# Kernel optimization log

Measured on AMD Instinct MI355X. Metric: run time of the kernel, lower is better.

## Reference

```python
import jax, jax.numpy as jnp
import numpy as np

B, L, IN, DM, DS, DC, EXP = 4, 1024, 256, 1024, 16, 4, 2
DI = EXP * DM            # d_inner = 2048
DTR = (DM + 15) // 16    # dt_rank = 64


def setup_inputs() -> dict:
    key = jax.random.key(0)
    ks = jax.random.split(key, 10)
    s = lambda k, sh, sc: jax.random.normal(k, sh, jnp.float32) * sc
    return {
        "x": s(ks[0], (B, L, IN), 1.0),
        "W_emb": s(ks[1], (DM, IN), IN ** -0.5),
        "b_emb": jnp.zeros((DM,), jnp.float32),
        "in_proj_w": s(ks[2], (2 * DI, DM), DM ** -0.5),
        "conv_w": s(ks[3], (DI, 1, DC), DC ** -0.5),
        "conv_b": jnp.zeros((DI,), jnp.float32),
        "x_proj_w": s(ks[4], (DTR + 2 * DS, DI), DI ** -0.5),
        "dt_proj_w": s(ks[5], (DI, DTR), DTR ** -0.5),
        "dt_proj_b": s(ks[6], (DI,), 0.1),
        "A_log": jnp.tile(jnp.log(jnp.arange(1, DS + 1, dtype=jnp.float32)), (DI, 1)),
        "D": jnp.ones((DI,), jnp.float32),
        "out_proj_w": s(ks[7], (DM, DI), DI ** -0.5),
        "fc_w": s(ks[8], (1, DM), DM ** -0.5),
        "fc_b": jnp.zeros((1,), jnp.float32),
    }


def _forward(x, W_emb, b_emb, in_proj_w, conv_w, conv_b, x_proj_w,
             dt_proj_w, dt_proj_b, A_log, D, out_proj_w, fc_w, fc_b):
    h = x @ W_emb.T + b_emb                      # [B,L,DM] input embedding
    xz = h @ in_proj_w.T                         # [B,L,2*DI]
    u, z = jnp.split(xz, 2, axis=-1)             # each [B,L,DI]
    # causal depthwise conv over time (pad left d_conv-1)
    uc = jax.lax.conv_general_dilated(
        u.transpose(0, 2, 1), conv_w, (1,), [(DC - 1, 0)],
        dimension_numbers=('NCH', 'OIH', 'NCH'), feature_group_count=DI)
    u = jax.nn.silu(uc.transpose(0, 2, 1) + conv_b)   # [B,L,DI]
    xdbl = u @ x_proj_w.T                        # [B,L,DTR+2*DS]
    dt, Bm, Cm = jnp.split(xdbl, [DTR, DTR + DS], axis=-1)
    delta = jax.nn.softplus(dt @ dt_proj_w.T + dt_proj_b)  # [B,L,DI]
    A = -jnp.exp(A_log)                          # [DI,DS]

    def step(hst, ins):
        d_t, B_t, C_t, u_t = ins                 # [B,DI],[B,DS],[B,DS],[B,DI]
        dA = jnp.exp(d_t[..., None] * A)         # [B,DI,DS]
        hst = dA * hst + (d_t * u_t)[..., None] * B_t[:, None, :]
        y = jnp.einsum('bds,bs->bd', hst, C_t)
        return hst, y

    h0 = jnp.zeros((B, DI, DS), u.dtype)
    _, ys = jax.lax.scan(step, h0, (delta.transpose(1, 0, 2),
                                    Bm.transpose(1, 0, 2),
                                    Cm.transpose(1, 0, 2),
                                    u.transpose(1, 0, 2)))
    y = ys.transpose(1, 0, 2) + D * u            # [B,L,DI] with D skip
    y = y * jax.nn.silu(z)                       # gate
    out = y @ out_proj_w.T                       # [B,L,DM]
    return out[:, -1, :] @ fc_w.T + fc_b         # [B,1]


def reference(x, W_emb, b_emb, in_proj_w, conv_w, conv_b, x_proj_w,
              dt_proj_w, dt_proj_b, A_log, D, out_proj_w, fc_w, fc_b):
    return _forward(x, W_emb, b_emb, in_proj_w, conv_w, conv_b, x_proj_w,
                    dt_proj_w, dt_proj_b, A_log, D, out_proj_w, fc_w, fc_b)
```

## Files before the change

### kernel.cpp

```cpp
#include <hip/hip_runtime.h>
#include <cstddef>
#include <cstdint>

namespace {

typedef _Float16 half8 __attribute__((ext_vector_type(8)));
typedef _Float16 half4 __attribute__((ext_vector_type(4)));
typedef float f32x4 __attribute__((ext_vector_type(4)));

constexpr int Bn   = 4;
constexpr int Ln   = 1024;
constexpr int INn  = 256;
constexpr int DMn  = 1024;
constexpr int DSn  = 16;
constexpr int DCn  = 4;
constexpr int DIn  = 2048;
constexpr int DTRn = 64;
constexpr int XPW  = DTRn + DSn;
constexpr int NCHUNK = 64;
constexpr int CHUNK  = Ln / NCHUNK;
constexpr int WCH  = 32;
constexpr int ML   = Bn * Ln;

__device__ __forceinline__ float silu_(float x) { return x / (1.f + __expf(-x)); }
__device__ __forceinline__ float softplus_(float x) {
    return fmaxf(x, 0.f) + __logf(1.f + __expf(-fabsf(x)));
}

__global__ __launch_bounds__(256)
void prep_mega(const float* __restrict__ x, _Float16* __restrict__ xh,
               const float* __restrict__ ip, _Float16* __restrict__ iph,
               const float* __restrict__ dtw, _Float16* __restrict__ dtwh,
               const float* __restrict__ W_emb, _Float16* __restrict__ W_embT,
               const float* __restrict__ x_proj, _Float16* __restrict__ xp_h,
               const float* __restrict__ fc_w, const float* __restrict__ out_w,
               float* __restrict__ wp,
               const float* __restrict__ b_emb, float* __restrict__ badd,
               const float* __restrict__ fc_b, float* __restrict__ out) {
    __shared__ float tile[32][33];
    const int bid = blockIdx.x, tid = threadIdx.x;
    if (bid < 4096) {
        const int n = bid;
        const float4 v = ((const float4*)ip)[n * 256 + tid];
        ((half4*)iph)[n * 256 + tid] =
            half4{(_Float16)v.x, (_Float16)v.y, (_Float16)v.z, (_Float16)v.w};
        const float4 bv = ((const float4*)b_emb)[tid];
        float s = v.x * bv.x + v.y * bv.y + v.z * bv.z + v.w * bv.w;
        for (int off = 32; off > 0; off >>= 1) s += __shfl_down(s, off);
        if ((tid & 63) == 0) tile[0][tid >> 6] = s;
        __syncthreads();
        if (tid == 0) badd[n] = tile[0][0] + tile[0][1] + tile[0][2] + tile[0][3];
    } else if (bid < 5248) {
        const float* in; _Float16* outp; int i;
        if (bid < 5120) { in = x;   outp = xh;   i = (bid - 4096) * 256 + tid; }
        else            { in = dtw; outp = dtwh; i = (bid - 5120) * 256 + tid; }
        const float4 v = ((const float4*)in)[i];
        ((half4*)outp)[i] = half4{(_Float16)v.x, (_Float16)v.y, (_Float16)v.z, (_Float16)v.w};
    } else if (bid < 5504) {
        const int bx = bid - 5248;
        const int m0 = (bx & 31) * 32, c0 = (bx >> 5) * 32;
        const int lc = tid & 31, lr = tid >> 5;
        #pragma unroll
        for (int ph = 0; ph < 4; ++ph)
            tile[lr + ph * 8][lc] = W_emb[(size_t)(m0 + lr + ph * 8) * INn + c0 + lc];
        __syncthreads();
        #pragma unroll
        for (int ph = 0; ph < 4; ++ph)
            W_embT[(size_t)(c0 + lr + ph * 8) * DMn + m0 + lc] = (_Float16)tile[lc][lr + ph * 8];
    } else if (bid < 5760) {
        const int i = (bid - 5504) * 256 + tid;
        const int r = i >> 9;
        const int c4 = i & 511;
        half4 h;
        if (r < XPW) {
            const float4 v = ((const float4*)(x_proj + (size_t)r * DIn))[c4];
            h = half4{(_Float16)v.x, (_Float16)v.y, (_Float16)v.z, (_Float16)v.w};
        } else {
            h = half4{(_Float16)0.f, (_Float16)0.f, (_Float16)0.f, (_Float16)0.f};
        }
        ((half4*)(xp_h + (size_t)r * DIn))[c4] = h;
    } else if (bid < 6016) {
        const int bx = bid - 5760;
        const int d = (bx & 7) * 256 + tid;
        const int c = bx >> 3;
        const int mstep = DMn / WCH;
        float s = 0.f;
        for (int m = c * mstep; m < (c + 1) * mstep; ++m)
            s += fc_w[m] * out_w[(size_t)m * DIn + d];
        wp[(size_t)c * DIn + d] = s;
    } else {
        if (tid < Bn) out[tid] = fc_b[0];
    }
}

__global__ __launch_bounds__(256)
void skgemm2(const _Float16* __restrict__ A, int lda,
             const _Float16* __restrict__ Bw, int ldb,
             float* __restrict__ P, int N, int Kc) {
    __shared__ _Float16 As[128 * 32];
    __shared__ _Float16 Bs[128 * 32];
    const int tid  = threadIdx.x;
    const int lane = tid & 63, wid = tid >> 6;
    const int wm = wid >> 1, wn = wid & 1;
    const int sk = blockIdx.x;
    const int m0 = blockIdx.y * 128;
    const int n0 = blockIdx.z * 128;
    const int M  = gridDim.y * 128;

    f32x4 acc[4][4] = {};
    const int kbeg = sk * Kc;
    for (int k0 = kbeg; k0 < kbeg + Kc; k0 += 32) {
        #pragma unroll
        for (int i = 0; i < 2; ++i) {
            const int off = tid * 16 + i * 4096;
            const int row = off >> 6;
            const int ch  = (off & 63) >> 1;
            __builtin_amdgcn_global_load_lds(
                (const __attribute__((address_space(1))) void*)(A + (size_t)(m0 + row) * lda + k0 + ch),
                (__attribute__((address_space(3))) void*)(&As[off >> 1]), 16, 0, 0);
            __builtin_amdgcn_global_load_lds(
                (const __attribute__((address_space(1))) void*)(Bw + (size_t)(n0 + row) * ldb + k0 + ch),
                (__attribute__((address_space(3))) void*)(&Bs[off >> 1]), 16, 0, 0);
        }
        __syncthreads();
        const int ar = lane & 15;
        const int kq = (lane >> 4) * 8;
        half8 af[4], bf[4];
        #pragma unroll
        for (int i = 0; i < 4; ++i)
            af[i] = *(const half8*)&As[(wm * 64 + i * 16 + ar) * 32 + kq];
        #pragma unroll
        for (int j = 0; j < 4; ++j)
            bf[j] = *(const half8*)&Bs[(wn * 64 + j * 16 + ar) * 32 + kq];
        #pragma unroll
        for (int i = 0; i < 4; ++i)
            #pragma unroll
            for (int j = 0; j < 4; ++j)
                acc[i][j] = __builtin_amdgcn_mfma_f32_16x16x32_f16(af[i], bf[j], acc[i][j], 0, 0, 0);
        __syncthreads();
    }
    const int cr = (lane >> 4) * 4;
    const int cn = lane & 15;
    #pragma unroll
    for (int i = 0; i < 4; ++i)
        #pragma unroll
        for (int j = 0; j < 4; ++j) {
            const int n = n0 + wn * 64 + j * 16 + cn;
            if (n < N) {
                #pragma unroll
                for (int r = 0; r < 4; ++r) {
                    const int m = m0 + wm * 64 + i * 16 + cr + r;
                    P[((size_t)sk * M + m) * N + n] = acc[i][j][r];
                }
            }
        }
}

__global__ __launch_bounds__(256)
void skcomb(const float* __restrict__ P, _Float16* __restrict__ out, int total, int nsk) {
    const int i = blockIdx.x * 256 + threadIdx.x;
    if (i >= total) return;
    float s = 0.f;
    for (int k = 0; k < nsk; ++k) s += P[(size_t)k * total + i];
    out[i] = (_Float16)s;
}

__global__ __launch_bounds__(256)
void skcombB_clast(const float* __restrict__ P, _Float16* __restrict__ dtBh,
                   const _Float16* __restrict__ u, const float* __restrict__ x_proj,
                   float* __restrict__ Clast) {
    const int bid = blockIdx.x, tid = threadIdx.x;
    if (bid < 1280) {
        const int i = bid * 256 + tid;
        float s = 0.f;
        #pragma unroll
        for (int k = 0; k < 8; ++k) s += P[(size_t)k * (ML * XPW) + i];
        dtBh[i] = (_Float16)s;
    } else {
        const int wave = tid >> 6, lane = tid & 63;
        const int task = (bid - 1280) * 4 + wave;
        const int s_idx = task & 15, b = task >> 4;
        const _Float16* ur = u + ((size_t)b * Ln + (Ln - 1)) * DIn;
        const float* w = x_proj + (size_t)(XPW + s_idx) * DIn;
        float s = 0.f;
        for (int k = lane; k < DIn; k += 64) s += (float)ur[k] * w[k];
        for (int off = 32; off > 0; off >>= 1) s += __shfl_down(s, off);
        if (lane == 0) Clast[b * DSn + s_idx] = s;
    }
}

__global__ __launch_bounds__(256)
void hgemm_upre(const _Float16* __restrict__ A, const _Float16* __restrict__ Bw,
                const float* __restrict__ bias, _Float16* __restrict__ Ch) {
    __shared__ _Float16 As[128 * 32];
    __shared__ _Float16 Bs[128 * 32];
    const int tid  = threadIdx.x;
    const int lane = tid & 63, wid = tid >> 6;
    const int wm = wid >> 1, wn = wid & 1;
    const int m0 = blockIdx.y * 128, n0 = blockIdx.x * 128;

    f32x4 acc[4][4] = {};
    for (int k0 = 0; k0 < INn; k0 += 32) {
        #pragma unroll
        for (int i = 0; i < 2; ++i) {
            const int off = tid * 16 + i * 4096;
            const int row = off >> 6;
            const int ch  = (off & 63) >> 1;
            __builtin_amdgcn_global_load_lds(
                (const __attribute__((address_space(1))) void*)(A + (size_t)(m0 + row) * INn + k0 + ch),
                (__attribute__((address_space(3))) void*)(&As[off >> 1]), 16, 0, 0);
            __builtin_amdgcn_global_load_lds(
                (const __attribute__((address_space(1))) void*)(Bw + (size_t)(n0 + row) * INn + k0 + ch),
                (__attribute__((address_space(3))) void*)(&Bs[off >> 1]), 16, 0, 0);
        }
        __syncthreads();
        const int ar = lane & 15;
        const int kq = (lane >> 4) * 8;
        half8 af[4], bf[4];
        #pragma unroll
        for (int i = 0; i < 4; ++i)
            af[i] = *(const half8*)&As[(wm * 64 + i * 16 + ar) * 32 + kq];
        #pragma unroll
        for (int j = 0; j < 4; ++j)
            bf[j] = *(const half8*)&Bs[(wn * 64 + j * 16 + ar) * 32 + kq];
        #pragma unroll
        for (int i = 0; i < 4; ++i)
            #pragma unroll
            for (int j = 0; j < 4; ++j)
                acc[i][j] = __builtin_amdgcn_mfma_f32_16x16x32_f16(af[i], bf[j], acc[i][j], 0, 0, 0);
        __syncthreads();
    }
    const int cr = (lane >> 4) * 4;
    const int cn = lane & 15;
    #pragma unroll
    for (int i = 0; i < 4; ++i)
        #pragma unroll
        for (int j = 0; j < 4; ++j) {
            const int n = n0 + wn * 64 + j * 16 + cn;
            #pragma unroll
            for (int r = 0; r < 4; ++r) {
                const int m = m0 + wm * 64 + i * 16 + cr + r;
                Ch[(size_t)m * DIn + n] = (_Float16)(acc[i][j][r] + bias[n]);
            }
        }
}

__global__ __launch_bounds__(256)
void conv_zlast(const _Float16* __restrict__ upre, const float* __restrict__ cw,
                const float* __restrict__ cb, _Float16* __restrict__ uh,
                const float* __restrict__ x, const _Float16* __restrict__ Wfh,
                const float* __restrict__ badd, float* __restrict__ zlast) {
    const int tid = threadIdx.x;
    const int bid = blockIdx.x;
    if (bid < 1024) {
        const int b  = bid >> 8;
        const int t0 = (bid & 255) * 4;
        const int d0 = tid * 8;
        const size_t rowbase = ((size_t)b * Ln + t0) * DIn + d0;
        half8 hzero;
        #pragma unroll
        for (int q = 0; q < 8; ++q) hzero[q] = (_Float16)0.f;
        half8 rows[7];
        if (t0 >= 3) {
            #pragma unroll
            for (int r = 0; r < 7; ++r)
                rows[r] = *(const half8*)(upre + rowbase + (ptrdiff_t)(r - 3) * DIn);
        } else {
            #pragma unroll
            for (int r = 0; r < 7; ++r) {
                const int t = t0 - 3 + r;
                rows[r] = (t >= 0) ? *(const half8*)(upre + rowbase + (ptrdiff_t)(r - 3) * DIn) : hzero;
            }
        }
        f32x4 cwq[8];
        float cbv[8];
        #pragma unroll
        for (int q = 0; q < 8; ++q) {
            cwq[q] = *(const f32x4*)(cw + (size_t)(d0 + q) * DCn);
            cbv[q] = cb[d0 + q];
        }
        #pragma unroll
        for (int s = 0; s < 4; ++s) {
            half8 o;
            #pragma unroll
            for (int q = 0; q < 8; ++q) {
                float acc = cbv[q];
                #pragma unroll
                for (int j = 0; j < DCn; ++j) acc += (float)rows[s + j][q] * cwq[q][j];
                o[q] = (_Float16)silu_(acc);
            }
            *(half8*)(uh + rowbase + (size_t)s * DIn) = o;
        }
    } else {
        const int t = (bid - 1024) * 256 + tid;
        const int j = t & (DIn - 1), b = t >> 11;
        const float4* x4 = (const float4*)(x + ((size_t)b * Ln + (Ln - 1)) * INn);
        const half4* w4 = (const half4*)(Wfh + (size_t)(DIn + j) * INn);
        float s = 0.f;
        #pragma unroll 8
        for (int q = 0; q < 64; ++q) {
            const float4 xv = x4[q];
            const half4 wv = w4[q];
            s += (float)wv[0] * xv.x + (float)wv[1] * xv.y
               + (float)wv[2] * xv.z + (float)wv[3] * xv.w;
        }
        zlast[(size_t)b * DIn + j] = s + badd[DIn + j];
    }
}

__global__ __launch_bounds__(256)
void delta_scan(const _Float16* __restrict__ dtBh, const _Float16* __restrict__ dtwh,
                const float* __restrict__ dt_b, const _Float16* __restrict__ uh,
                const float* __restrict__ A_log,
                float* __restrict__ cS, _Float16* __restrict__ cH) {
    __shared__ _Float16 As[128 * 32];
    __shared__ _Float16 Bs[128 * 32];
    __shared__ _Float16 Ds[128][132];
    const int tid = threadIdx.x;
    const int lane = tid & 63, wid = tid >> 6;
    const int wm = wid >> 1, wn = wid & 1;
    const int m0 = blockIdx.y * 128, n0 = blockIdx.x * 128;

    f32x4 acc[4][4] = {};
    for (int k0 = 0; k0 < DTRn; k0 += 32) {
        #pragma unroll
        for (int i = 0; i < 2; ++i) {
            const int off = tid * 16 + i * 4096;
            const int row = off >> 6;
            const int ch  = (off & 63) >> 1;
            __builtin_amdgcn_global_load_lds(
                (const __attribute__((address_space(1))) void*)(dtBh + (size_t)(m0 + row) * XPW + k0 + ch),
                (__attribute__((address_space(3))) void*)(&As[off >> 1]), 16, 0, 0);
            __builtin_amdgcn_global_load_lds(
                (const __attribute__((address_space(1))) void*)(dtwh + (size_t)(n0 + row) * DTRn + k0 + ch),
                (__attribute__((address_space(3))) void*)(&Bs[off >> 1]), 16, 0, 0);
        }
        __syncthreads();
        const int ar = lane & 15;
        const int kq = (lane >> 4) * 8;
        half8 af[4], bf[4];
        #pragma unroll
        for (int i = 0; i < 4; ++i)
            af[i] = *(const half8*)&As[(wm * 64 + i * 16 + ar) * 32 + kq];
        #pragma unroll
        for (int j = 0; j < 4; ++j)
            bf[j] = *(const half8*)&Bs[(wn * 64 + j * 16 + ar) * 32 + kq];
        #pragma unroll
        for (int i = 0; i < 4; ++i)
            #pragma unroll
            for (int j = 0; j < 4; ++j)
                acc[i][j] = __builtin_amdgcn_mfma_f32_16x16x32_f16(af[i], bf[j], acc[i][j], 0, 0, 0);
        __syncthreads();
    }

    {
        const int row = tid >> 1, off = (tid & 1) * 8;
        *(half8*)&Bs[row * 16 + off] =
            *(const half8*)(dtBh + (size_t)(m0 + row) * XPW + 64 + off);
    }
    {
        const int cr = (lane >> 4) * 4;
        const int cn = lane & 15;
        #pragma unroll
        for (int i = 0; i < 4; ++i)
            #pragma unroll
            for (int j = 0; j < 4; ++j) {
                const int ln = wn * 64 + j * 16 + cn;
                const float bb = dt_b[n0 + ln];
                #pragma unroll
                for (int r = 0; r < 4; ++r) {
                    const int lm = wm * 64 + i * 16 + cr + r;
                    Ds[lm][ln] = (_Float16)softplus_(acc[i][j][r] + bb);
                }
            }
    }
    __syncthreads();

    const int bb = m0 >> 10;
    const int tb = m0 & 1023;
    const int dcol = tid & 127;
    const int d = n0 + dcol;
    float A[DSn];
    {
        const float4* al = (const float4*)(A_log + (size_t)d * DSn);
        #pragma unroll
        for (int q = 0; q < 4; ++q) {
            const float4 v = al[q];
            A[q * 4 + 0] = -__expf(v.x); A[q * 4 + 1] = -__expf(v.y);
            A[q * 4 + 2] = -__expf(v.z); A[q * 4 + 3] = -__expf(v.w);
        }
    }
    const float A0 = A[0];
    bool structured = true;
    #pragma unroll
    for (int s = 1; s < DSn; ++s)
        structured = structured && (fabsf(A[s] - (float)(s + 1) * A0) <= 1e-4f * (s + 1));

    for (int ci = (tid >> 7); ci < 8; ci += 2) {
        float h[DSn];
        #pragma unroll
        for (int s = 0; s < DSn; ++s) h[s] = 0.f;
        float Ssum = 0.f;
        const size_t ubase = ((size_t)bb * Ln + tb + ci * 16) * DIn + d;
        if (structured) {
            for (int tt = 0; tt < CHUNK; ++tt) {
                const int lr = ci * 16 + tt;
                const float dl = (float)Ds[lr][dcol];
                const float uu = (float)uh[ubase + (size_t)tt * DIn];
                const float du = dl * uu;
                Ssum += dl;
                const half8 bv0 = *(const half8*)&Bs[lr * 16];
                const half8 bv1 = *(const half8*)&Bs[lr * 16 + 8];
                float Bv[DSn];
                #pragma unroll
                for (int q = 0; q < 8; ++q) { Bv[q] = (float)bv0[q]; Bv[8 + q] = (float)bv1[q]; }
                const float e1 = __expf(dl * A0);
                const float e2 = e1 * e1, e4 = e2 * e2, e8 = e4 * e4;
                float E[DSn];
                E[0] = e1;      E[1] = e2;      E[2] = e2 * e1;  E[3] = e4;
                E[4] = e4 * e1; E[5] = e4 * e2; E[6] = E[5] * e1; E[7] = e8;
                E[8] = e8 * e1; E[9] = e8 * e2; E[10] = E[9] * e1; E[11] = e8 * e4;
                E[12] = E[11] * e1; E[13] = E[11] * e2; E[14] = E[13] * e1; E[15] = e8 * e8;
                #pragma unroll
                for (int s = 0; s < DSn; ++s) h[s] = E[s] * h[s] + du * Bv[s];
            }
        } else {
            for (int tt = 0; tt < CHUNK; ++tt) {
                const int lr = ci * 16 + tt;
                const float dl = (float)Ds[lr][dcol];
                const float uu = (float)uh[ubase + (size_t)tt * DIn];
                const float du = dl * uu;
                Ssum += dl;
                const half8 bv0 = *(const half8*)&Bs[lr * 16];
                const half8 bv1 = *(const half8*)&Bs[lr * 16 + 8];
                float Bv[DSn];
                #pragma unroll
                for (int q = 0; q < 8; ++q) { Bv[q] = (float)bv0[q]; Bv[8 + q] = (float)bv1[q]; }
                #pragma unroll
                for (int s = 0; s < DSn; ++s) h[s] = __expf(dl * A[s]) * h[s] + du * Bv[s];
            }
        }
        const int c = (tb >> 4) + ci;
        const size_t cidx = ((size_t)bb * NCHUNK + c) * DIn + d;
        cS[cidx] = Ssum;
        half8 o0, o1;
        #pragma unroll
        for (int q = 0; q < 8; ++q) { o0[q] = (_Float16)h[q]; o1[q] = (_Float16)h[8 + q]; }
        *(half8*)(cH + cidx * DSn) = o0;
        *(half8*)(cH + cidx * DSn + 8) = o1;
    }
}

__global__ __launch_bounds__(256)
void combine_v3(const float* __restrict__ cS, const _Float16* __restrict__ cH,
                const float* __restrict__ A_log, const float* __restrict__ Clast,
                const float* __restrict__ Dp, const _Float16* __restrict__ u,
                const float* __restrict__ zlast, const float* __restrict__ wp,
                float* __restrict__ out) {
    __shared__ float acc[16];
    const int tid = threadIdx.x;
    const int s = tid & 15;
    const int d = blockIdx.x * 16 + (tid >> 4);
    const int b = blockIdx.y;
    const float A = -__expf(A_log[(size_t)d * DSn + s]);
    float h = 0.f;
    const size_t cb0 = (size_t)b * NCHUNK;
    for (int c = 0; c < NCHUNK; ++c) {
        const size_t cidx = (cb0 + c) * DIn + d;
        h = __expf(A * cS[cidx]) * h + (float)cH[cidx * DSn + s];
    }
    float y = h * Clast[b * DSn + s];
    y += __shfl_xor(y, 1);
    y += __shfl_xor(y, 2);
    y += __shfl_xor(y, 4);
    y += __shfl_xor(y, 8);
    if (s == 0) {
        const float ul = (float)u[((size_t)b * Ln + (Ln - 1)) * DIn + d];
        float yy = y + Dp[d] * ul;
        yy *= silu_(zlast[(size_t)b * DIn + d]);
        float w = 0.f;
        #pragma unroll
        for (int c = 0; c < WCH; ++c) w += wp[(size_t)c * DIn + d];
        acc[tid >> 4] = yy * w;
    }
    __syncthreads();
    if (tid == 0) {
        float t = 0.f;
        #pragma unroll
        for (int i = 0; i < 16; ++i) t += acc[i];
        atomicAdd(&out[b], t);
    }
}

}

extern "C" void kernel_launch(void* const* d_in, const int* in_sizes, int n_in,
                              void* d_out, int out_size, void* d_ws, size_t ws_size,
                              hipStream_t stream) {
    (void)in_sizes; (void)n_in; (void)out_size; (void)ws_size;
    const float* x       = (const float*)d_in[0];
    const float* W_emb   = (const float*)d_in[1];
    const float* b_emb   = (const float*)d_in[2];
    const float* in_proj = (const float*)d_in[3];
    const float* conv_w  = (const float*)d_in[4];
    const float* conv_b  = (const float*)d_in[5];
    const float* x_proj  = (const float*)d_in[6];
    const float* dt_w    = (const float*)d_in[7];
    const float* dt_b    = (const float*)d_in[8];
    const float* A_log   = (const float*)d_in[9];
    const float* Dp      = (const float*)d_in[10];
    const float* out_w   = (const float*)d_in[11];
    const float* fc_w    = (const float*)d_in[12];
    const float* fc_b    = (const float*)d_in[13];
    float* out = (float*)d_out;
    char* w8 = (char*)d_ws;

    const size_t MB = 1ull << 20;
    _Float16* upreh    = (_Float16*)(w8);
    _Float16* uh       = (_Float16*)(w8 + 16 * MB);
    float*    wfoldP   = (float*)(w8 + 32 * MB);
    float*    skp      = (float*)(w8 + 48 * MB);
    float*    cS       = skp;
    _Float16* cH       = (_Float16*)(w8 + 50 * MB);
    _Float16* dtBh     = (_Float16*)(w8 + 67 * MB);
    _Float16* xh       = (_Float16*)(w8 + 68 * MB);
    _Float16* W_embT_h = (_Float16*)(w8 + 70 * MB);
    _Float16* in_projh = (_Float16*)(w8 + 71 * MB);
    _Float16* xp_h     = (_Float16*)(w8 + 79 * MB);
    _Float16* dt_wh    = (_Float16*)(w8 + 80 * MB);
    _Float16* Wfoldh   = (_Float16*)(w8 + 81 * MB);
    float*    wp       = (float*)(w8 + 83 * MB);
    float*    badd     = (float*)(w8 + 84 * MB);
    float*    zlast    = badd + 4096;
    float*    Clast    = zlast + (size_t)Bn * DIn;

    prep_mega<<<6017, 256, 0, stream>>>(x, xh, in_proj, in_projh, dt_w, dt_wh,
                                        W_emb, W_embT_h, x_proj, xp_h,
                                        fc_w, out_w, wp, b_emb, badd, fc_b, out);
    skgemm2<<<dim3(4, ML / 128, 2), 256, 0, stream>>>(
        in_projh, DMn, W_embT_h, DMn, wfoldP, INn, 256);
    skcomb<<<(ML * INn + 255) / 256, 256, 0, stream>>>(wfoldP, Wfoldh, ML * INn, 4);
    hgemm_upre<<<dim3(DIn / 128, ML / 128), 256, 0, stream>>>(xh, Wfoldh, badd, upreh);
    conv_zlast<<<1056, 256, 0, stream>>>(upreh, conv_w, conv_b, uh, x, Wfoldh, badd, zlast);
    skgemm2<<<dim3(8, ML / 128, 1), 256, 0, stream>>>(uh, DIn, xp_h, DIn, skp, XPW, 256);
    skcombB_clast<<<1296, 256, 0, stream>>>(skp, dtBh, uh, x_proj, Clast);
    delta_scan<<<dim3(DIn / 128, ML / 128), 256, 0, stream>>>(
        dtBh, dt_wh, dt_b, uh, A_log, cS, cH);
    combine_v3<<<dim3(DIn / 16, Bn), 256, 0, stream>>>(
        cS, cH, A_log, Clast, Dp, uh, zlast, wp, out);
}
```

Baseline: 130.2 us.

## Fuse upre GEMM with causal conv and split delta GEMM from scan

```diff
diff --git a/kernel.cpp b/kernel.cpp
--- a/kernel.cpp
+++ b/kernel.cpp
@@ -190,112 +190,17 @@
 }
 
 __global__ __launch_bounds__(256)
-void hgemm_upre(const _Float16* __restrict__ A, const _Float16* __restrict__ Bw,
-                const float* __restrict__ bias, _Float16* __restrict__ Ch) {
-    __shared__ _Float16 As[128 * 32];
-    __shared__ _Float16 Bs[128 * 32];
-    const int tid  = threadIdx.x;
-    const int lane = tid & 63, wid = tid >> 6;
-    const int wm = wid >> 1, wn = wid & 1;
-    const int m0 = blockIdx.y * 128, n0 = blockIdx.x * 128;
-
-    f32x4 acc[4][4] = {};
-    for (int k0 = 0; k0 < INn; k0 += 32) {
-        #pragma unroll
-        for (int i = 0; i < 2; ++i) {
-            const int off = tid * 16 + i * 4096;
-            const int row = off >> 6;
-            const int ch  = (off & 63) >> 1;
-            __builtin_amdgcn_global_load_lds(
-                (const __attribute__((address_space(1))) void*)(A + (size_t)(m0 + row) * INn + k0 + ch),
-                (__attribute__((address_space(3))) void*)(&As[off >> 1]), 16, 0, 0);
-            __builtin_amdgcn_global_load_lds(
-                (const __attribute__((address_space(1))) void*)(Bw + (size_t)(n0 + row) * INn + k0 + ch),
-                (__attribute__((address_space(3))) void*)(&Bs[off >> 1]), 16, 0, 0);
-        }
-        __syncthreads();
-        const int ar = lane & 15;
-        const int kq = (lane >> 4) * 8;
-        half8 af[4], bf[4];
-        #pragma unroll
-        for (int i = 0; i < 4; ++i)
-            af[i] = *(const half8*)&As[(wm * 64 + i * 16 + ar) * 32 + kq];
-        #pragma unroll
-        for (int j = 0; j < 4; ++j)
-            bf[j] = *(const half8*)&Bs[(wn * 64 + j * 16 + ar) * 32 + kq];
-        #pragma unroll
-        for (int i = 0; i < 4; ++i)
-            #pragma unroll
-            for (int j = 0; j < 4; ++j)
-                acc[i][j] = __builtin_amdgcn_mfma_f32_16x16x32_f16(af[i], bf[j], acc[i][j], 0, 0, 0);
-        __syncthreads();
-    }
-    const int cr = (lane >> 4) * 4;
-    const int cn = lane & 15;
-    #pragma unroll
-    for (int i = 0; i < 4; ++i)
-        #pragma unroll
-        for (int j = 0; j < 4; ++j) {
-            const int n = n0 + wn * 64 + j * 16 + cn;
-            #pragma unroll
-            for (int r = 0; r < 4; ++r) {
-                const int m = m0 + wm * 64 + i * 16 + cr + r;
-                Ch[(size_t)m * DIn + n] = (_Float16)(acc[i][j][r] + bias[n]);
-            }
-        }
-}
-
-__global__ __launch_bounds__(256)
-void conv_zlast(const _Float16* __restrict__ upre, const float* __restrict__ cw,
-                const float* __restrict__ cb, _Float16* __restrict__ uh,
-                const float* __restrict__ x, const _Float16* __restrict__ Wfh,
-                const float* __restrict__ badd, float* __restrict__ zlast) {
+void upre_conv_zlast(const _Float16* __restrict__ xh, const _Float16* __restrict__ Wfoldh,
+                     const float* __restrict__ badd,
+                     const float* __restrict__ cw, const float* __restrict__ cb,
+                     _Float16* __restrict__ uh,
+                     const float* __restrict__ x, float* __restrict__ zlast) {
     const int tid = threadIdx.x;
-    const int bid = blockIdx.x;
-    if (bid < 1024) {
-        const int b  = bid >> 8;
-        const int t0 = (bid & 255) * 4;
-        const int d0 = tid * 8;
-        const size_t rowbase = ((size_t)b * Ln + t0) * DIn + d0;
-        half8 hzero;
-        #pragma unroll
-        for (int q = 0; q < 8; ++q) hzero[q] = (_Float16)0.f;
-        half8 rows[7];
-        if (t0 >= 3) {
-            #pragma unroll
-            for (int r = 0; r < 7; ++r)
-                rows[r] = *(const half8*)(upre + rowbase + (ptrdiff_t)(r - 3) * DIn);
-        } else {
-            #pragma unroll
-            for (int r = 0; r < 7; ++r) {
-                const int t = t0 - 3 + r;
-                rows[r] = (t >= 0) ? *(const half8*)(upre + rowbase + (ptrdiff_t)(r - 3) * DIn) : hzero;
-            }
-        }
-        f32x4 cwq[8];
-        float cbv[8];
-        #pragma unroll
-        for (int q = 0; q < 8; ++q) {
-            cwq[q] = *(const f32x4*)(cw + (size_t)(d0 + q) * DCn);
-            cbv[q] = cb[d0 + q];
-        }
-        #pragma unroll
-        for (int s = 0; s < 4; ++s) {
-            half8 o;
-            #pragma unroll
-            for (int q = 0; q < 8; ++q) {
-                float acc = cbv[q];
-                #pragma unroll
-                for (int j = 0; j < DCn; ++j) acc += (float)rows[s + j][q] * cwq[q][j];
-                o[q] = (_Float16)silu_(acc);
-            }
-            *(half8*)(uh + rowbase + (size_t)s * DIn) = o;
-        }
-    } else {
-        const int t = (bid - 1024) * 256 + tid;
+    if (blockIdx.x == 16) {
+        const int t = blockIdx.y * 256 + tid;
         const int j = t & (DIn - 1), b = t >> 11;
         const float4* x4 = (const float4*)(x + ((size_t)b * Ln + (Ln - 1)) * INn);
-        const half4* w4 = (const half4*)(Wfh + (size_t)(DIn + j) * INn);
+        const half4* w4 = (const half4*)(Wfoldh + (size_t)(DIn + j) * INn);
         float s = 0.f;
         #pragma unroll 8
         for (int q = 0; q < 64; ++q) {
@@ -305,35 +210,42 @@
                + (float)wv[2] * xv.z + (float)wv[3] * xv.w;
         }
         zlast[(size_t)b * DIn + j] = s + badd[DIn + j];
-    }
-}
-
-__global__ __launch_bounds__(256)
-void delta_scan(const _Float16* __restrict__ dtBh, const _Float16* __restrict__ dtwh,
-                const float* __restrict__ dt_b, const _Float16* __restrict__ uh,
-                const float* __restrict__ A_log,
-                float* __restrict__ cS, _Float16* __restrict__ cH) {
-    __shared__ _Float16 As[128 * 32];
-    __shared__ _Float16 Bs[128 * 32];
-    __shared__ _Float16 Ds[128][132];
-    const int tid = threadIdx.x;
+        return;
+    }
+    __shared__ _Float16 smem[144 * 132];
+    _Float16* As = smem;
+    _Float16* Bs = smem + 144 * 32;
+    _Float16 (*Ds)[132] = (_Float16 (*)[132])smem;
+
     const int lane = tid & 63, wid = tid >> 6;
     const int wm = wid >> 1, wn = wid & 1;
     const int m0 = blockIdx.y * 128, n0 = blockIdx.x * 128;
 
     f32x4 acc[4][4] = {};
-    for (int k0 = 0; k0 < DTRn; k0 += 32) {
+    f32x4 acch[4] = {};
+    for (int k0 = 0; k0 < INn; k0 += 32) {
         #pragma unroll
         for (int i = 0; i < 2; ++i) {
             const int off = tid * 16 + i * 4096;
             const int row = off >> 6;
             const int ch  = (off & 63) >> 1;
-            __builtin_amdgcn_global_load_lds(
-                (const __attribute__((address_space(1))) void*)(dtBh + (size_t)(m0 + row) * XPW + k0 + ch),
+            int srow = m0 - 16 + row;
+            if (srow < 0) srow = 0;
+            __builtin_amdgcn_global_load_lds(
+                (const __attribute__((address_space(1))) void*)(xh + (size_t)srow * INn + k0 + ch),
                 (__attribute__((address_space(3))) void*)(&As[off >> 1]), 16, 0, 0);
-            __builtin_amdgcn_global_load_lds(
-                (const __attribute__((address_space(1))) void*)(dtwh + (size_t)(n0 + row) * DTRn + k0 + ch),
+            const _Float16* gb = Wfoldh + (size_t)(n0 + row) * INn + k0 + ch;
+            __builtin_amdgcn_global_load_lds(
+                (const __attribute__((address_space(1))) void*)gb,
                 (__attribute__((address_space(3))) void*)(&Bs[off >> 1]), 16, 0, 0);
+        }
+        if (tid < 64) {
+            const int off = tid * 16 + 8192;
+            const int row = off >> 6;
+            const int ch  = (off & 63) >> 1;
+            __builtin_amdgcn_global_load_lds(
+                (const __attribute__((address_space(1))) void*)(xh + (size_t)(m0 - 16 + row) * INn + k0 + ch),
+                (__attribute__((address_space(3))) void*)(&As[off >> 1]), 16, 0, 0);
         }
         __syncthreads();
         const int ar = lane & 15;
@@ -341,7 +253,7 @@
         half8 af[4], bf[4];
         #pragma unroll
         for (int i = 0; i < 4; ++i)
-            af[i] = *(const half8*)&As[(wm * 64 + i * 16 + ar) * 32 + kq];
+            af[i] = *(const half8*)&As[(16 + wm * 64 + i * 16 + ar) * 32 + kq];
         #pragma unroll
         for (int j = 0; j < 4; ++j)
             bf[j] = *(const half8*)&Bs[(wn * 64 + j * 16 + ar) * 32 + kq];
@@ -350,14 +262,15 @@
             #pragma unroll
             for (int j = 0; j < 4; ++j)
                 acc[i][j] = __builtin_amdgcn_mfma_f32_16x16x32_f16(af[i], bf[j], acc[i][j], 0, 0, 0);
-        __syncthreads();
-    }
-
-    {
-        const int row = tid >> 1, off = (tid & 1) * 8;
-        *(half8*)&Bs[row * 16 + off] =
-            *(const half8*)(dtBh + (size_t)(m0 + row) * XPW + 64 + off);
-    }
+        if (wm == 0) {
+            const half8 afh = *(const half8*)&As[ar * 32 + kq];
+            #pragma unroll
+            for (int j = 0; j < 4; ++j)
+                acch[j] = __builtin_amdgcn_mfma_f32_16x16x32_f16(afh, bf[j], acch[j], 0, 0, 0);
+        }
+        __syncthreads();
+    }
+
     {
         const int cr = (lane >> 4) * 4;
         const int cn = lane & 15;
@@ -365,90 +278,183 @@
         for (int i = 0; i < 4; ++i)
             #pragma unroll
             for (int j = 0; j < 4; ++j) {
-                const int ln = wn * 64 + j * 16 + cn;
-                const float bb = dt_b[n0 + ln];
+                const int col = wn * 64 + j * 16 + cn;
+                const float bb = badd[n0 + col];
                 #pragma unroll
-                for (int r = 0; r < 4; ++r) {
-                    const int lm = wm * 64 + i * 16 + cr + r;
-                    Ds[lm][ln] = (_Float16)softplus_(acc[i][j][r] + bb);
-                }
+                for (int r = 0; r < 4; ++r)
+                    Ds[16 + wm * 64 + i * 16 + cr + r][col] = (_Float16)(acc[i][j][r] + bb);
             }
+        if (wm == 0) {
+            #pragma unroll
+            for (int j = 0; j < 4; ++j) {
+                const int col = wn * 64 + j * 16 + cn;
+                const float bb = badd[n0 + col];
+                #pragma unroll
+                for (int r = 0; r < 4; ++r)
+                    Ds[cr + r][col] = (_Float16)(acch[j][r] + bb);
+            }
+        }
     }
     __syncthreads();
 
-    const int bb = m0 >> 10;
-    const int tb = m0 & 1023;
-    const int dcol = tid & 127;
-    const int d = n0 + dcol;
-    float A[DSn];
-    {
-        const float4* al = (const float4*)(A_log + (size_t)d * DSn);
-        #pragma unroll
-        for (int q = 0; q < 4; ++q) {
-            const float4 v = al[q];
-            A[q * 4 + 0] = -__expf(v.x); A[q * 4 + 1] = -__expf(v.y);
-            A[q * 4 + 2] = -__expf(v.z); A[q * 4 + 3] = -__expf(v.w);
-        }
+    const int col8 = tid & 15;
+    const int d0l = col8 * 8;
+    f32x4 cwq[8];
+    float cbv[8];
+    #pragma unroll
+    for (int q = 0; q < 8; ++q) {
+        cwq[q] = *(const f32x4*)(cw + (size_t)(n0 + d0l + q) * DCn);
+        cbv[q] = cb[n0 + d0l + q];
+    }
+    const int b  = m0 >> 10;
+    const int t0 = m0 & 1023;
+    half8 hzero;
+    #pragma unroll
+    for (int q = 0; q < 8; ++q) hzero[q] = (_Float16)0.f;
+    for (int k = 0; k < 8; ++k) {
+        const int rr = (tid >> 4) + k * 16;
+        half8 w[4];
+        #pragma unroll
+        for (int jj = 0; jj < 4; ++jj) {
+            const int dr = 16 + rr - 3 + jj;
+            w[jj] = ((t0 == 0) && (dr < 16)) ? hzero : *(const half8*)&Ds[dr][d0l];
+        }
+        half8 o;
+        #pragma unroll
+        for (int q = 0; q < 8; ++q) {
+            float a = cbv[q];
+            #pragma unroll
+            for (int jj = 0; jj < 4; ++jj) a += (float)w[jj][q] * cwq[q][jj];
+            o[q] = (_Float16)silu_(a);
+        }
+        *(half8*)(uh + ((size_t)b * Ln + t0 + rr) * DIn + n0 + d0l) = o;
+    }
+}
+
+__global__ __launch_bounds__(256)
+void hgemm_delta(const _Float16* __restrict__ A, const _Float16* __restrict__ Bw,
+                 const float* __restrict__ bias, _Float16* __restrict__ Ch) {
+    __shared__ _Float16 As[128 * 32];
+    __shared__ _Float16 Bs[128 * 32];
+    const int tid  = threadIdx.x;
+    const int lane = tid & 63, wid = tid >> 6;
+    const int wm = wid >> 1, wn = wid & 1;
+    const int m0 = blockIdx.y * 128, n0 = blockIdx.x * 128;
+
+    f32x4 acc[4][4] = {};
+    for (int k0 = 0; k0 < DTRn; k0 += 32) {
+        #pragma unroll
+        for (int i = 0; i < 2; ++i) {
+            const int off = tid * 16 + i * 4096;
+            const int row = off >> 6;
+            const int ch  = (off & 63) >> 1;
+            __builtin_amdgcn_global_load_lds(
+                (const __attribute__((address_space(1))) void*)(A + (size_t)(m0 + row) * XPW + k0 + ch),
+                (__attribute__((address_space(3))) void*)(&As[off >> 1]), 16, 0, 0);
+            __builtin_amdgcn_global_load_lds(
+                (const __attribute__((address_space(1))) void*)(Bw + (size_t)(n0 + row) * DTRn + k0 + ch),
+                (__attribute__((address_space(3))) void*)(&Bs[off >> 1]), 16, 0, 0);
+        }
+        __syncthreads();
+        const int ar = lane & 15;
+        const int kq = (lane >> 4) * 8;
+        half8 af[4], bf[4];
+        #pragma unroll
+        for (int i = 0; i < 4; ++i)
+            af[i] = *(const half8*)&As[(wm * 64 + i * 16 + ar) * 32 + kq];
+        #pragma unroll
+        for (int j = 0; j < 4; ++j)
+            bf[j] = *(const half8*)&Bs[(wn * 64 + j * 16 + ar) * 32 + kq];
+        #pragma unroll
+        for (int i = 0; i < 4; ++i)
+            #pragma unroll
+            for (int j = 0; j < 4; ++j)
+                acc[i][j] = __builtin_amdgcn_mfma_f32_16x16x32_f16(af[i], bf[j], acc[i][j], 0, 0, 0);
+        __syncthreads();
+    }
+    const int cr = (lane >> 4) * 4;
+    const int cn = lane & 15;
+    #pragma unroll
+    for (int i = 0; i < 4; ++i)
+        #pragma unroll
+        for (int j = 0; j < 4; ++j) {
+            const int n = n0 + wn * 64 + j * 16 + cn;
+            #pragma unroll
+            for (int r = 0; r < 4; ++r) {
+                const int m = m0 + wm * 64 + i * 16 + cr + r;
+                Ch[(size_t)m * DIn + n] = (_Float16)softplus_(acc[i][j][r] + bias[n]);
+            }
+        }
+}
+
+__global__ __launch_bounds__(256)
+void scan_chunk_kernel(const _Float16* __restrict__ delta, const _Float16* __restrict__ u,
+                       const _Float16* __restrict__ dtBh, const float* __restrict__ A_log,
+                       float* __restrict__ cS, _Float16* __restrict__ cH) {
+    const int d = blockIdx.x * 256 + threadIdx.x;
+    const int c = blockIdx.y, b = blockIdx.z;
+    float A[DSn], h[DSn];
+    const float4* al = (const float4*)(A_log + (size_t)d * DSn);
+    #pragma unroll
+    for (int q = 0; q < 4; ++q) {
+        const float4 v = al[q];
+        A[q * 4 + 0] = -__expf(v.x); A[q * 4 + 1] = -__expf(v.y);
+        A[q * 4 + 2] = -__expf(v.z); A[q * 4 + 3] = -__expf(v.w);
+        h[q * 4 + 0] = 0.f; h[q * 4 + 1] = 0.f; h[q * 4 + 2] = 0.f; h[q * 4 + 3] = 0.f;
     }
     const float A0 = A[0];
     bool structured = true;
     #pragma unroll
     for (int s = 1; s < DSn; ++s)
         structured = structured && (fabsf(A[s] - (float)(s + 1) * A0) <= 1e-4f * (s + 1));
-
-    for (int ci = (tid >> 7); ci < 8; ci += 2) {
-        float h[DSn];
-        #pragma unroll
-        for (int s = 0; s < DSn; ++s) h[s] = 0.f;
-        float Ssum = 0.f;
-        const size_t ubase = ((size_t)bb * Ln + tb + ci * 16) * DIn + d;
-        if (structured) {
-            for (int tt = 0; tt < CHUNK; ++tt) {
-                const int lr = ci * 16 + tt;
-                const float dl = (float)Ds[lr][dcol];
-                const float uu = (float)uh[ubase + (size_t)tt * DIn];
-                const float du = dl * uu;
-                Ssum += dl;
-                const half8 bv0 = *(const half8*)&Bs[lr * 16];
-                const half8 bv1 = *(const half8*)&Bs[lr * 16 + 8];
-                float Bv[DSn];
-                #pragma unroll
-                for (int q = 0; q < 8; ++q) { Bv[q] = (float)bv0[q]; Bv[8 + q] = (float)bv1[q]; }
-                const float e1 = __expf(dl * A0);
-                const float e2 = e1 * e1, e4 = e2 * e2, e8 = e4 * e4;
-                float E[DSn];
-                E[0] = e1;      E[1] = e2;      E[2] = e2 * e1;  E[3] = e4;
-                E[4] = e4 * e1; E[5] = e4 * e2; E[6] = E[5] * e1; E[7] = e8;
-                E[8] = e8 * e1; E[9] = e8 * e2; E[10] = E[9] * e1; E[11] = e8 * e4;
-                E[12] = E[11] * e1; E[13] = E[11] * e2; E[14] = E[13] * e1; E[15] = e8 * e8;
-                #pragma unroll
-                for (int s = 0; s < DSn; ++s) h[s] = E[s] * h[s] + du * Bv[s];
-            }
-        } else {
-            for (int tt = 0; tt < CHUNK; ++tt) {
-                const int lr = ci * 16 + tt;
-                const float dl = (float)Ds[lr][dcol];
-                const float uu = (float)uh[ubase + (size_t)tt * DIn];
-                const float du = dl * uu;
-                Ssum += dl;
-                const half8 bv0 = *(const half8*)&Bs[lr * 16];
-                const half8 bv1 = *(const half8*)&Bs[lr * 16 + 8];
-                float Bv[DSn];
-                #pragma unroll
-                for (int q = 0; q < 8; ++q) { Bv[q] = (float)bv0[q]; Bv[8 + q] = (float)bv1[q]; }
-                #pragma unroll
-                for (int s = 0; s < DSn; ++s) h[s] = __expf(dl * A[s]) * h[s] + du * Bv[s];
-            }
-        }
-        const int c = (tb >> 4) + ci;
-        const size_t cidx = ((size_t)bb * NCHUNK + c) * DIn + d;
-        cS[cidx] = Ssum;
-        half8 o0, o1;
-        #pragma unroll
-        for (int q = 0; q < 8; ++q) { o0[q] = (_Float16)h[q]; o1[q] = (_Float16)h[8 + q]; }
-        *(half8*)(cH + cidx * DSn) = o0;
-        *(half8*)(cH + cidx * DSn + 8) = o1;
-    }
+    float Ssum = 0.f;
+    const size_t base = ((size_t)b * Ln + (size_t)c * CHUNK) * DIn + d;
+    const _Float16* Bp = dtBh + ((size_t)b * Ln + (size_t)c * CHUNK) * XPW + DTRn;
+    if (structured) {
+        #pragma unroll 4
+        for (int tt = 0; tt < CHUNK; ++tt) {
+            const float dl = (float)delta[base + (size_t)tt * DIn];
+            const float uu = (float)u[base + (size_t)tt * DIn];
+            const float du = dl * uu;
+            Ssum += dl;
+            const half8 bv0 = *(const half8*)(Bp + tt * XPW);
+            const half8 bv1 = *(const half8*)(Bp + tt * XPW + 8);
+            float Bv[DSn];
+            #pragma unroll
+            for (int q = 0; q < 8; ++q) { Bv[q] = (float)bv0[q]; Bv[8 + q] = (float)bv1[q]; }
+            const float e1 = __expf(dl * A0);
+            const float e2 = e1 * e1, e4 = e2 * e2, e8 = e4 * e4;
+            float E[DSn];
+            E[0] = e1;      E[1] = e2;      E[2] = e2 * e1;  E[3] = e4;
+            E[4] = e4 * e1; E[5] = e4 * e2; E[6] = E[5] * e1; E[7] = e8;
+            E[8] = e8 * e1; E[9] = e8 * e2; E[10] = E[9] * e1; E[11] = e8 * e4;
+            E[12] = E[11] * e1; E[13] = E[11] * e2; E[14] = E[13] * e1; E[15] = e8 * e8;
+            #pragma unroll
+            for (int s = 0; s < DSn; ++s) h[s] = E[s] * h[s] + du * Bv[s];
+        }
+    } else {
+        #pragma unroll 4
+        for (int tt = 0; tt < CHUNK; ++tt) {
+            const float dl = (float)delta[base + (size_t)tt * DIn];
+            const float uu = (float)u[base + (size_t)tt * DIn];
+            const float du = dl * uu;
+            Ssum += dl;
+            const half8 bv0 = *(const half8*)(Bp + tt * XPW);
+            const half8 bv1 = *(const half8*)(Bp + tt * XPW + 8);
+            float Bv[DSn];
+            #pragma unroll
+            for (int q = 0; q < 8; ++q) { Bv[q] = (float)bv0[q]; Bv[8 + q] = (float)bv1[q]; }
+            #pragma unroll
+            for (int s = 0; s < DSn; ++s) h[s] = __expf(dl * A[s]) * h[s] + du * Bv[s];
+        }
+    }
+    const size_t cidx = ((size_t)b * NCHUNK + c) * DIn + d;
+    cS[cidx] = Ssum;
+    half8 o0, o1;
+    #pragma unroll
+    for (int q = 0; q < 8; ++q) { o0[q] = (_Float16)h[q]; o1[q] = (_Float16)h[8 + q]; }
+    *(half8*)(cH + cidx * DSn) = o0;
+    *(half8*)(cH + cidx * DSn + 8) = o1;
 }
 
 __global__ __launch_bounds__(256)
@@ -516,9 +522,9 @@
     char* w8 = (char*)d_ws;
 
     const size_t MB = 1ull << 20;
-    _Float16* upreh    = (_Float16*)(w8);
     _Float16* uh       = (_Float16*)(w8 + 16 * MB);
     float*    wfoldP   = (float*)(w8 + 32 * MB);
+    _Float16* deltah   = (_Float16*)(w8 + 32 * MB);
     float*    skp      = (float*)(w8 + 48 * MB);
     float*    cS       = skp;
     _Float16* cH       = (_Float16*)(w8 + 50 * MB);
@@ -540,12 +546,13 @@
     skgemm2<<<dim3(4, ML / 128, 2), 256, 0, stream>>>(
         in_projh, DMn, W_embT_h, DMn, wfoldP, INn, 256);
     skcomb<<<(ML * INn + 255) / 256, 256, 0, stream>>>(wfoldP, Wfoldh, ML * INn, 4);
-    hgemm_upre<<<dim3(DIn / 128, ML / 128), 256, 0, stream>>>(xh, Wfoldh, badd, upreh);
-    conv_zlast<<<1056, 256, 0, stream>>>(upreh, conv_w, conv_b, uh, x, Wfoldh, badd, zlast);
+    upre_conv_zlast<<<dim3(17, ML / 128), 256, 0, stream>>>(
+        xh, Wfoldh, badd, conv_w, conv_b, uh, x, zlast);
     skgemm2<<<dim3(8, ML / 128, 1), 256, 0, stream>>>(uh, DIn, xp_h, DIn, skp, XPW, 256);
     skcombB_clast<<<1296, 256, 0, stream>>>(skp, dtBh, uh, x_proj, Clast);
-    delta_scan<<<dim3(DIn / 128, ML / 128), 256, 0, stream>>>(
-        dtBh, dt_wh, dt_b, uh, A_log, cS, cH);
+    hgemm_delta<<<dim3(DIn / 128, ML / 128), 256, 0, stream>>>(dtBh, dt_wh, dt_b, deltah);
+    scan_chunk_kernel<<<dim3(DIn / 256, NCHUNK, Bn), 256, 0, stream>>>(
+        deltah, uh, dtBh, A_log, cS, cH);
     combine_v3<<<dim3(DIn / 16, Bn), 256, 0, stream>>>(
         cS, cH, A_log, Clast, Dp, uh, zlast, wp, out);
 }
```

Measured after the change: 124.6 us. 4.3% less time.
